# Kernel tuning notes

Measured on AMD Instinct MI355X. Metric: run time of the kernel, lower is better.

Reference implementation:

```python
import jax, jax.numpy as jnp
import numpy as np

# irreps_in == irreps_out == 512x0e + 256x1o + 128x2e
# each entry: (multiplicity, irrep dimension 2l+1)
IRREPS = [(512, 1), (256, 3), (128, 5)]
DIM_TOTAL = sum(m * d for m, d in IRREPS)          # 1920
WEIGHT_NUMEL = sum(m * m for m, _ in IRREPS)       # 344064
N = 16384


def setup_inputs() -> dict:
    key = jax.random.key(0)
    kx, kw = jax.random.split(key)
    x = jax.random.normal(kx, (N, DIM_TOTAL), dtype=jnp.float32)
    weight = jax.random.normal(kw, (WEIGHT_NUMEL,), dtype=jnp.float32)
    return {"x": x, "weight": weight}


def reference(x, weight):
    """Segmented (block-diagonal per irrep) linear mixing with 1/sqrt(fan_in) norm."""
    n = x.shape[0]
    outs = []
    x_off = 0
    w_off = 0
    for mul, d in IRREPS:
        seg = x[:, x_off:x_off + mul * d].reshape(n, mul, d)      # [N, mul, 2l+1]
        W = weight[w_off:w_off + mul * mul].reshape(mul, mul)     # [mul_in, mul_out]
        scale = jnp.asarray(1.0 / np.sqrt(mul), dtype=x.dtype)
        y = jnp.einsum('nui,uv->nvi', seg, W) * scale             # channel mix per component
        outs.append(y.reshape(n, mul * d))
        x_off += mul * d
        w_off += mul * mul
    return jnp.concatenate(outs, axis=-1)
```

## Files before the change

### kernel.cpp

```cpp
#include <hip/hip_runtime.h>


typedef float  f32x4  __attribute__((ext_vector_type(4)));
typedef short  bf16x8 __attribute__((ext_vector_type(8)));

#define ROWLEN 1920

__device__ __forceinline__ unsigned short f2bf(float f) {
    union { float f; unsigned int u; } c; c.f = f;
    unsigned int u = c.u;
    u += 0x7fffu + ((u >> 16) & 1u);
    return (unsigned short)(u >> 16);
}

__global__ __launch_bounds__(256) void prep_weights(const float* __restrict__ w,
                                                    unsigned short* __restrict__ wt) {
    int g = blockIdx.x * 256 + threadIdx.x;
    if (g >= 344064) return;
    int base, sh;
    if      (g < 262144) { base = 0;      sh = 9; }
    else if (g < 327680) { base = 262144; sh = 8; }
    else                 { base = 327680; sh = 7; }
    int local = g - base;
    int u = local >> sh;
    int v = local & ((1 << sh) - 1);
    wt[base + (v << sh) + u] = f2bf(w[g]);
}

template<int MUL, int D, int TN, int X_OFF, int WT_BASE>
__device__ __forceinline__ void seg_body(const int bid,
                                         const float* __restrict__ x,
                                         const unsigned short* __restrict__ wt,
                                         float* __restrict__ out,
                                         const float scale,
                                         unsigned short* lds) {
    constexpr int KB      = 32;
    constexpr int NSTEP   = MUL / KB;
    constexpr int M_LOG   = TN * D;
    constexpr int MT      = M_LOG / 16;
    constexpr int WAVE_NT = MUL / 64;
    constexpr int ST      = MUL + 8;
    constexpr int ROW_F4  = MUL * D / 4;
    constexpr int ITERS   = TN * ROW_F4 / 256;

    const int tid  = threadIdx.x;
    const int wave = tid >> 6;
    const int lane = tid & 63;
    const int q    = lane >> 4;
    const int t16  = lane & 15;
    const int n0   = bid * TN;

    const float* __restrict__ xblk = x + X_OFF + n0 * ROWLEN;

#pragma unroll 4
    for (int it = 0; it < ITERS; ++it) {
        const int idx = tid + it * 256;
        const int nl  = idx / ROW_F4;
        const int c4  = (idx - nl * ROW_F4) * 4;
        const f32x4 vv = *(const f32x4*)(xblk + nl * ROWLEN + c4);
        if (D == 1) {
            unsigned int lo = (unsigned int)f2bf(vv[0]) | ((unsigned int)f2bf(vv[1]) << 16);
            unsigned int hi = (unsigned int)f2bf(vv[2]) | ((unsigned int)f2bf(vv[3]) << 16);
            unsigned int* p = (unsigned int*)&lds[nl * ST + c4];
            p[0] = lo; p[1] = hi;
        } else {
#pragma unroll
            for (int e = 0; e < 4; ++e) {
                const int c = c4 + e;
                const int u = c / D;
                const int i = c - u * D;
                lds[(i * TN + nl) * ST + u] = f2bf(vv[e]);
            }
        }
    }

    f32x4 acc[MT][WAVE_NT];
#pragma unroll
    for (int a = 0; a < MT; ++a)
#pragma unroll
        for (int b = 0; b < WAVE_NT; ++b) acc[a][b] = (f32x4)0.0f;

    __syncthreads();

    const unsigned short* __restrict__ wblk = wt + WT_BASE;
    const int vbase = wave * (WAVE_NT * 16) + t16;

#pragma unroll 1
    for (int ks = 0; ks < NSTEP; ++ks) {
        bf16x8 afr[MT];
#pragma unroll
        for (int tm = 0; tm < MT; ++tm)
            afr[tm] = *(const bf16x8*)&lds[(16 * tm + t16) * ST + ks * KB + q * 8];
#pragma unroll
        for (int tv = 0; tv < WAVE_NT; ++tv) {
            const bf16x8 bfr = *(const bf16x8*)&wblk[(vbase + tv * 16) * MUL + ks * KB + q * 8];
#pragma unroll
            for (int tm = 0; tm < MT; ++tm)
                acc[tm][tv] = __builtin_amdgcn_mfma_f32_16x16x32_bf16(afr[tm], bfr, acc[tm][tv], 0, 0, 0);
        }
    }

#pragma unroll
    for (int tm = 0; tm < MT; ++tm) {
#pragma unroll
        for (int tv = 0; tv < WAVE_NT; ++tv) {
            const int v = vbase + tv * 16;
#pragma unroll
            for (int r = 0; r < 4; ++r) {
                const int rit  = q * 4 + r;
                const int lrow = 16 * tm + rit;
                const int i    = lrow / TN;
                const int nl   = lrow - i * TN;
                out[(n0 + nl) * ROWLEN + X_OFF + v * D + i] = acc[tm][tv][r] * scale;
            }
        }
    }
}

__global__ __launch_bounds__(256, 4) void fused_gemm(const float* __restrict__ x,
                                                     const unsigned short* __restrict__ wt,
                                                     float* __restrict__ out) {
    extern __shared__ unsigned short lds[];
    const int b = blockIdx.x;
    const int g = b / 5;
    const int r = b - g * 5;
    if (r == 0) {
        seg_body<512, 1, 32, 0, 0>(g, x, wt, out, 0.044194173824f, lds);
    } else if (r <= 2) {
        seg_body<256, 3, 16, 512, 262144>(g * 2 + (r - 1), x, wt, out, 0.0625f, lds);
    } else {
        seg_body<128, 5, 16, 1280, 327680>(g * 2 + (r - 3), x, wt, out, 0.088388347648f, lds);
    }
}

extern "C" void kernel_launch(void* const* d_in, const int* in_sizes, int n_in,
                              void* d_out, int out_size, void* d_ws, size_t ws_size,
                              hipStream_t stream) {
    const float* x = (const float*)d_in[0];
    const float* w = (const float*)d_in[1];
    float* out = (float*)d_out;
    unsigned short* wt = (unsigned short*)d_ws;

    hipLaunchKernelGGL(prep_weights, dim3((344064 + 255) / 256), dim3(256), 0, stream, w, wt);
    hipLaunchKernelGGL(fused_gemm, dim3(2560), dim3(256), 33280, stream, x, wt, out);
}
```

Measured before the change: 283.7 us.

## Pre-swizzle weights into MFMA fragment order and software-pipeline the K loop

The weight prep kernel now writes bf16 weights in the exact per-lane MFMA B-fragment order, so each lane in the GEMM loads one contiguous 16-byte chunk per tile instead of doing strided transposed reads. The K loop is double-buffered in registers: the next step's A and B fragments are loaded while the current MFMAs issue. The scalar segment tile shrinks from 32 to 16 rows, giving a uniform 3-block grouping, a larger grid and less LDS per block. This raises register pressure and halves weight reuse per block for the 0e segment.

```diff
diff --git a/kernel.cpp b/kernel.cpp
--- a/kernel.cpp
+++ b/kernel.cpp
@@ -15,16 +15,23 @@
 
 __global__ __launch_bounds__(256) void prep_weights(const float* __restrict__ w,
                                                     unsigned short* __restrict__ wt) {
-    int g = blockIdx.x * 256 + threadIdx.x;
-    if (g >= 344064) return;
-    int base, sh;
-    if      (g < 262144) { base = 0;      sh = 9; }
-    else if (g < 327680) { base = 262144; sh = 8; }
-    else                 { base = 327680; sh = 7; }
-    int local = g - base;
-    int u = local >> sh;
-    int v = local & ((1 << sh) - 1);
-    wt[base + (v << sh) + u] = f2bf(w[g]);
+    const int g = blockIdx.x * 256 + threadIdx.x;
+    if (g >= 43008) return;
+    int t, base, mul, lognstep;
+    if      (g < 32768) { t = g;         base = 0;      mul = 512; lognstep = 4; }
+    else if (g < 40960) { t = g - 32768; base = 262144; mul = 256; lognstep = 3; }
+    else                { t = g - 40960; base = 327680; mul = 128; lognstep = 2; }
+    const int lane = t & 63;
+    const int rest = t >> 6;
+    const int ks   = rest & ((1 << lognstep) - 1);
+    const int vt   = rest >> lognstep;
+    const int v    = vt * 16 + (lane & 15);
+    const int k0   = ks * 32 + (lane >> 4) * 8;
+    const float* __restrict__ src = w + base + k0 * mul + v;
+    bf16x8 vv;
+#pragma unroll
+    for (int j = 0; j < 8; ++j) vv[j] = (short)f2bf(src[j * mul]);
+    *(bf16x8*)&wt[base + t * 8] = vv;
 }
 
 template<int MUL, int D, int TN, int X_OFF, int WT_BASE>
@@ -42,6 +49,7 @@
     constexpr int ST      = MUL + 8;
     constexpr int ROW_F4  = MUL * D / 4;
     constexpr int ITERS   = TN * ROW_F4 / 256;
+    constexpr int TVS     = NSTEP * 512;
 
     const int tid  = threadIdx.x;
     const int wave = tid >> 6;
@@ -51,8 +59,21 @@
     const int n0   = bid * TN;
 
     const float* __restrict__ xblk = x + X_OFF + n0 * ROWLEN;
+    const unsigned short* __restrict__ wfrag =
+        wt + WT_BASE + (wave * WAVE_NT) * TVS + lane * 8;
 
-#pragma unroll 4
+    f32x4 acc[MT][WAVE_NT];
+#pragma unroll
+    for (int a = 0; a < MT; ++a)
+#pragma unroll
+        for (int b = 0; b < WAVE_NT; ++b) acc[a][b] = (f32x4)0.0f;
+
+    bf16x8 bfr[WAVE_NT];
+#pragma unroll
+    for (int tv = 0; tv < WAVE_NT; ++tv)
+        bfr[tv] = *(const bf16x8*)&wfrag[tv * TVS];
+
+#pragma unroll
     for (int it = 0; it < ITERS; ++it) {
         const int idx = tid + it * 256;
         const int nl  = idx / ROW_F4;
@@ -74,37 +95,43 @@
         }
     }
 
-    f32x4 acc[MT][WAVE_NT];
-#pragma unroll
-    for (int a = 0; a < MT; ++a)
-#pragma unroll
-        for (int b = 0; b < WAVE_NT; ++b) acc[a][b] = (f32x4)0.0f;
-
     __syncthreads();
 
-    const unsigned short* __restrict__ wblk = wt + WT_BASE;
-    const int vbase = wave * (WAVE_NT * 16) + t16;
+    bf16x8 afr[MT];
+#pragma unroll
+    for (int tm = 0; tm < MT; ++tm)
+        afr[tm] = *(const bf16x8*)&lds[(16 * tm + t16) * ST + q * 8];
 
-#pragma unroll 1
-    for (int ks = 0; ks < NSTEP; ++ks) {
-        bf16x8 afr[MT];
+#pragma unroll 2
+    for (int ks = 0; ks < NSTEP - 1; ++ks) {
+        bf16x8 bnx[WAVE_NT], anx[MT];
+#pragma unroll
+        for (int tv = 0; tv < WAVE_NT; ++tv)
+            bnx[tv] = *(const bf16x8*)&wfrag[tv * TVS + (ks + 1) * 512];
 #pragma unroll
         for (int tm = 0; tm < MT; ++tm)
-            afr[tm] = *(const bf16x8*)&lds[(16 * tm + t16) * ST + ks * KB + q * 8];
+            anx[tm] = *(const bf16x8*)&lds[(16 * tm + t16) * ST + (ks + 1) * KB + q * 8];
 #pragma unroll
-        for (int tv = 0; tv < WAVE_NT; ++tv) {
-            const bf16x8 bfr = *(const bf16x8*)&wblk[(vbase + tv * 16) * MUL + ks * KB + q * 8];
+        for (int tv = 0; tv < WAVE_NT; ++tv)
 #pragma unroll
             for (int tm = 0; tm < MT; ++tm)
-                acc[tm][tv] = __builtin_amdgcn_mfma_f32_16x16x32_bf16(afr[tm], bfr, acc[tm][tv], 0, 0, 0);
-        }
+                acc[tm][tv] = __builtin_amdgcn_mfma_f32_16x16x32_bf16(afr[tm], bfr[tv], acc[tm][tv], 0, 0, 0);
+#pragma unroll
+        for (int tv = 0; tv < WAVE_NT; ++tv) bfr[tv] = bnx[tv];
+#pragma unroll
+        for (int tm = 0; tm < MT; ++tm) afr[tm] = anx[tm];
     }
+#pragma unroll
+    for (int tv = 0; tv < WAVE_NT; ++tv)
+#pragma unroll
+        for (int tm = 0; tm < MT; ++tm)
+            acc[tm][tv] = __builtin_amdgcn_mfma_f32_16x16x32_bf16(afr[tm], bfr[tv], acc[tm][tv], 0, 0, 0);
 
 #pragma unroll
     for (int tm = 0; tm < MT; ++tm) {
 #pragma unroll
         for (int tv = 0; tv < WAVE_NT; ++tv) {
-            const int v = vbase + tv * 16;
+            const int v = wave * (WAVE_NT * 16) + t16 + tv * 16;
 #pragma unroll
             for (int r = 0; r < 4; ++r) {
                 const int rit  = q * 4 + r;
@@ -122,14 +149,14 @@
                                                      float* __restrict__ out) {
     extern __shared__ unsigned short lds[];
     const int b = blockIdx.x;
-    const int g = b / 5;
-    const int r = b - g * 5;
+    const int g = b / 3;
+    const int r = b - g * 3;
     if (r == 0) {
-        seg_body<512, 1, 32, 0, 0>(g, x, wt, out, 0.044194173824f, lds);
-    } else if (r <= 2) {
-        seg_body<256, 3, 16, 512, 262144>(g * 2 + (r - 1), x, wt, out, 0.0625f, lds);
+        seg_body<512, 1, 16, 0, 0>(g, x, wt, out, 0.044194173824f, lds);
+    } else if (r == 1) {
+        seg_body<256, 3, 16, 512, 262144>(g, x, wt, out, 0.0625f, lds);
     } else {
-        seg_body<128, 5, 16, 1280, 327680>(g * 2 + (r - 3), x, wt, out, 0.088388347648f, lds);
+        seg_body<128, 5, 16, 1280, 327680>(g, x, wt, out, 0.088388347648f, lds);
     }
 }
 
@@ -141,6 +168,6 @@
     float* out = (float*)d_out;
     unsigned short* wt = (unsigned short*)d_ws;
 
-    hipLaunchKernelGGL(prep_weights, dim3((344064 + 255) / 256), dim3(256), 0, stream, w, wt);
-    hipLaunchKernelGGL(fused_gemm, dim3(2560), dim3(256), 33280, stream, x, wt, out);
+    hipLaunchKernelGGL(prep_weights, dim3(168), dim3(256), 0, stream, w, wt);
+    hipLaunchKernelGGL(fused_gemm, dim3(3072), dim3(256), 25344, stream, x, wt, out);
 }
```

Result: faster. 251.6 us (-11.3%).

## Pre-swizzle weights into MFMA fragment order, use 8 waves, prefetch B fragments

Applied to the files above, without the earlier changes.

The weight prep kernel now writes bf16 weights in per-lane MFMA fragment order, so each wave's B-operand load is a contiguous 16-byte-per-lane read. Blocks grow from 4 to 8 waves, which halves the output columns each wave handles. B fragments are loaded into registers before the x tile is staged to LDS, so the global weight latency overlaps the staging. When a wave's fragments fit they are all kept in registers; otherwise a 3-deep software prefetch is used. The trade-off is higher register pressure at 512 threads with launch_bounds(512,4), and occupancy may drop.

```diff
diff --git a/kernel.cpp b/kernel.cpp
--- a/kernel.cpp
+++ b/kernel.cpp
@@ -15,16 +15,21 @@
 
 __global__ __launch_bounds__(256) void prep_weights(const float* __restrict__ w,
                                                     unsigned short* __restrict__ wt) {
-    int g = blockIdx.x * 256 + threadIdx.x;
+    const int g = blockIdx.x * 256 + threadIdx.x;
     if (g >= 344064) return;
-    int base, sh;
-    if      (g < 262144) { base = 0;      sh = 9; }
-    else if (g < 327680) { base = 262144; sh = 8; }
-    else                 { base = 327680; sh = 7; }
-    int local = g - base;
-    int u = local >> sh;
-    int v = local & ((1 << sh) - 1);
-    wt[base + (v << sh) + u] = f2bf(w[g]);
+    int base, lmul;
+    if      (g < 262144) { base = 0;      lmul = 9; }
+    else if (g < 327680) { base = 262144; lmul = 8; }
+    else                 { base = 327680; lmul = 7; }
+    const int local = g - base;
+    const int u = local >> lmul;
+    const int v = local & ((1 << lmul) - 1);
+    const int nstep_log = lmul - 5;
+    const int vt   = v >> 4;
+    const int ks   = u >> 5;
+    const int lane = (((u >> 3) & 3) << 4) | (v & 15);
+    const int j    = u & 7;
+    wt[base + ((((vt << nstep_log) + ks) << 6) + lane) * 8 + j] = f2bf(w[g]);
 }
 
 template<int MUL, int D, int TN, int X_OFF, int WT_BASE>
@@ -38,10 +43,13 @@
     constexpr int NSTEP   = MUL / KB;
     constexpr int M_LOG   = TN * D;
     constexpr int MT      = M_LOG / 16;
-    constexpr int WAVE_NT = MUL / 64;
+    constexpr int NWAVE   = 8;
+    constexpr int WAVE_NT = MUL / (NWAVE * 16);
     constexpr int ST      = MUL + 8;
     constexpr int ROW_F4  = MUL * D / 4;
-    constexpr int ITERS   = TN * ROW_F4 / 256;
+    constexpr int ITERS   = TN * ROW_F4 / (NWAVE * 64);
+    constexpr int TVS     = NSTEP * 512;
+    constexpr bool BREG   = (WAVE_NT * NSTEP) <= 16;
 
     const int tid  = threadIdx.x;
     const int wave = tid >> 6;
@@ -51,28 +59,8 @@
     const int n0   = bid * TN;
 
     const float* __restrict__ xblk = x + X_OFF + n0 * ROWLEN;
-
-#pragma unroll 4
-    for (int it = 0; it < ITERS; ++it) {
-        const int idx = tid + it * 256;
-        const int nl  = idx / ROW_F4;
-        const int c4  = (idx - nl * ROW_F4) * 4;
-        const f32x4 vv = *(const f32x4*)(xblk + nl * ROWLEN + c4);
-        if (D == 1) {
-            unsigned int lo = (unsigned int)f2bf(vv[0]) | ((unsigned int)f2bf(vv[1]) << 16);
-            unsigned int hi = (unsigned int)f2bf(vv[2]) | ((unsigned int)f2bf(vv[3]) << 16);
-            unsigned int* p = (unsigned int*)&lds[nl * ST + c4];
-            p[0] = lo; p[1] = hi;
-        } else {
-#pragma unroll
-            for (int e = 0; e < 4; ++e) {
-                const int c = c4 + e;
-                const int u = c / D;
-                const int i = c - u * D;
-                lds[(i * TN + nl) * ST + u] = f2bf(vv[e]);
-            }
-        }
-    }
+    const unsigned short* __restrict__ wfrag =
+        wt + WT_BASE + (wave * WAVE_NT) * TVS + lane * 8;
 
     f32x4 acc[MT][WAVE_NT];
 #pragma unroll
@@ -80,23 +68,77 @@
 #pragma unroll
         for (int b = 0; b < WAVE_NT; ++b) acc[a][b] = (f32x4)0.0f;
 
-    __syncthreads();
+    auto stage_tile = [&]() {
+#pragma unroll
+        for (int it = 0; it < ITERS; ++it) {
+            const int idx = tid + it * (NWAVE * 64);
+            const int nl  = idx / ROW_F4;
+            const int c4  = (idx - nl * ROW_F4) * 4;
+            const f32x4 vv = *(const f32x4*)(xblk + nl * ROWLEN + c4);
+            if (D == 1) {
+                unsigned int lo = (unsigned int)f2bf(vv[0]) | ((unsigned int)f2bf(vv[1]) << 16);
+                unsigned int hi = (unsigned int)f2bf(vv[2]) | ((unsigned int)f2bf(vv[3]) << 16);
+                unsigned int* p = (unsigned int*)&lds[nl * ST + c4];
+                p[0] = lo; p[1] = hi;
+            } else {
+#pragma unroll
+                for (int e = 0; e < 4; ++e) {
+                    const int c = c4 + e;
+                    const int u = c / D;
+                    const int i = c - u * D;
+                    lds[(i * TN + nl) * ST + u] = f2bf(vv[e]);
+                }
+            }
+        }
+    };
 
-    const unsigned short* __restrict__ wblk = wt + WT_BASE;
-    const int vbase = wave * (WAVE_NT * 16) + t16;
-
-#pragma unroll 1
-    for (int ks = 0; ks < NSTEP; ++ks) {
-        bf16x8 afr[MT];
+    if constexpr (BREG) {
+        bf16x8 breg[WAVE_NT * NSTEP];
 #pragma unroll
-        for (int tm = 0; tm < MT; ++tm)
-            afr[tm] = *(const bf16x8*)&lds[(16 * tm + t16) * ST + ks * KB + q * 8];
+        for (int tv = 0; tv < WAVE_NT; ++tv)
 #pragma unroll
-        for (int tv = 0; tv < WAVE_NT; ++tv) {
-            const bf16x8 bfr = *(const bf16x8*)&wblk[(vbase + tv * 16) * MUL + ks * KB + q * 8];
+            for (int ks = 0; ks < NSTEP; ++ks)
+                breg[tv * NSTEP + ks] = *(const bf16x8*)&wfrag[tv * TVS + ks * 512];
+        stage_tile();
+        __syncthreads();
+#pragma unroll
+        for (int ks = 0; ks < NSTEP; ++ks) {
+            bf16x8 afr[MT];
 #pragma unroll
             for (int tm = 0; tm < MT; ++tm)
-                acc[tm][tv] = __builtin_amdgcn_mfma_f32_16x16x32_bf16(afr[tm], bfr, acc[tm][tv], 0, 0, 0);
+                afr[tm] = *(const bf16x8*)&lds[(16 * tm + t16) * ST + ks * KB + q * 8];
+#pragma unroll
+            for (int tv = 0; tv < WAVE_NT; ++tv)
+#pragma unroll
+                for (int tm = 0; tm < MT; ++tm)
+                    acc[tm][tv] = __builtin_amdgcn_mfma_f32_16x16x32_bf16(afr[tm], breg[tv * NSTEP + ks], acc[tm][tv], 0, 0, 0);
+        }
+    } else {
+        constexpr int PF = 3;
+        bf16x8 bfr[4][WAVE_NT];
+#pragma unroll
+        for (int p = 0; p < PF; ++p)
+#pragma unroll
+            for (int tv = 0; tv < WAVE_NT; ++tv)
+                bfr[p][tv] = *(const bf16x8*)&wfrag[tv * TVS + p * 512];
+        stage_tile();
+        __syncthreads();
+#pragma unroll
+        for (int ks = 0; ks < NSTEP; ++ks) {
+            if (ks + PF < NSTEP) {
+#pragma unroll
+                for (int tv = 0; tv < WAVE_NT; ++tv)
+                    bfr[(ks + PF) & 3][tv] = *(const bf16x8*)&wfrag[tv * TVS + (ks + PF) * 512];
+            }
+            bf16x8 afr[MT];
+#pragma unroll
+            for (int tm = 0; tm < MT; ++tm)
+                afr[tm] = *(const bf16x8*)&lds[(16 * tm + t16) * ST + ks * KB + q * 8];
+#pragma unroll
+            for (int tv = 0; tv < WAVE_NT; ++tv)
+#pragma unroll
+                for (int tm = 0; tm < MT; ++tm)
+                    acc[tm][tv] = __builtin_amdgcn_mfma_f32_16x16x32_bf16(afr[tm], bfr[ks & 3][tv], acc[tm][tv], 0, 0, 0);
         }
     }
 
@@ -104,7 +146,7 @@
     for (int tm = 0; tm < MT; ++tm) {
 #pragma unroll
         for (int tv = 0; tv < WAVE_NT; ++tv) {
-            const int v = vbase + tv * 16;
+            const int v = wave * (WAVE_NT * 16) + t16 + tv * 16;
 #pragma unroll
             for (int r = 0; r < 4; ++r) {
                 const int rit  = q * 4 + r;
@@ -117,7 +159,7 @@
     }
 }
 
-__global__ __launch_bounds__(256, 4) void fused_gemm(const float* __restrict__ x,
+__global__ __launch_bounds__(512, 4) void fused_gemm(const float* __restrict__ x,
                                                      const unsigned short* __restrict__ wt,
                                                      float* __restrict__ out) {
     extern __shared__ unsigned short lds[];
@@ -141,6 +183,6 @@
     float* out = (float*)d_out;
     unsigned short* wt = (unsigned short*)d_ws;
 
-    hipLaunchKernelGGL(prep_weights, dim3((344064 + 255) / 256), dim3(256), 0, stream, w, wt);
-    hipLaunchKernelGGL(fused_gemm, dim3(2560), dim3(256), 33280, stream, x, wt, out);
+    hipLaunchKernelGGL(prep_weights, dim3(1344), dim3(256), 0, stream, w, wt);
+    hipLaunchKernelGGL(fused_gemm, dim3(2560), dim3(512), 33280, stream, x, wt, out);
 }
```

After: 235.8 us. 1.2x faster.

## Double-buffer K-sliced A/B tiles in LDS with async global-to-LDS weight loads

Applied to the files above, without the earlier changes.

Restructures the fused segmented GEMM into a K-step pipeline. Each 32-wide K slice of x (converted to bf16) and of the weights is staged into double-buffered LDS, so the next slice loads while the current one feeds MFMA. Weights are pre-swizzled into an MFMA-fragment-major layout and copied with global_load_lds. The kernel also moves to 512-thread blocks with a 2D wave tiling, larger row tiles and N-blocking, giving a different grid decomposition. This adds a barrier per K step and more LDS per block (48 KB), which may reduce occupancy.

```diff
diff --git a/kernel.cpp b/kernel.cpp
--- a/kernel.cpp
+++ b/kernel.cpp
@@ -13,123 +13,171 @@
     return (unsigned short)(u >> 16);
 }
 
+__device__ __forceinline__ void gload_lds16(const unsigned short* g, unsigned short* l) {
+    __builtin_amdgcn_global_load_lds(
+        (const __attribute__((address_space(1))) unsigned int*)g,
+        (__attribute__((address_space(3))) unsigned int*)l, 16, 0, 0);
+}
+
 __global__ __launch_bounds__(256) void prep_weights(const float* __restrict__ w,
                                                     unsigned short* __restrict__ wt) {
-    int g = blockIdx.x * 256 + threadIdx.x;
+    const int g = blockIdx.x * 256 + threadIdx.x;
     if (g >= 344064) return;
-    int base, sh;
-    if      (g < 262144) { base = 0;      sh = 9; }
-    else if (g < 327680) { base = 262144; sh = 8; }
-    else                 { base = 327680; sh = 7; }
-    int local = g - base;
-    int u = local >> sh;
-    int v = local & ((1 << sh) - 1);
-    wt[base + (v << sh) + u] = f2bf(w[g]);
+    int base, lmul;
+    if      (g < 262144) { base = 0;      lmul = 9; }
+    else if (g < 327680) { base = 262144; lmul = 8; }
+    else                 { base = 327680; lmul = 7; }
+    const int local = g - base;
+    const int u = local >> lmul;
+    const int v = local & ((1 << lmul) - 1);
+    const int NSUB = 1 << (lmul - 4);
+    const int ks   = u >> 5;
+    const int nsub = v >> 4;
+    const int lane = (((u >> 3) & 3) << 4) | (v & 15);
+    const int j    = u & 7;
+    wt[base + ((ks * NSUB + nsub) * 64 + lane) * 8 + j] = f2bf(w[g]);
 }
 
-template<int MUL, int D, int TN, int X_OFF, int WT_BASE>
-__device__ __forceinline__ void seg_body(const int bid,
+template<int MUL, int D, int TN, int BN, int X_OFF, int WT_BASE, int WROWS>
+__device__ __forceinline__ void seg_body(const int wid,
                                          const float* __restrict__ x,
                                          const unsigned short* __restrict__ wt,
                                          float* __restrict__ out,
                                          const float scale,
                                          unsigned short* lds) {
-    constexpr int KB      = 32;
-    constexpr int NSTEP   = MUL / KB;
-    constexpr int M_LOG   = TN * D;
-    constexpr int MT      = M_LOG / 16;
-    constexpr int WAVE_NT = MUL / 64;
-    constexpr int ST      = MUL + 8;
-    constexpr int ROW_F4  = MUL * D / 4;
-    constexpr int ITERS   = TN * ROW_F4 / 256;
+    constexpr int NSTEP    = MUL / 32;
+    constexpr int M_LOG    = TN * D;
+    constexpr int WCOLS    = 8 / WROWS;
+    constexpr int MT       = M_LOG / (16 * WROWS);
+    constexpr int NT       = BN / (16 * WCOLS);
+    constexpr int NSUB_WG  = BN / 16;
+    constexpr int NSUB_SEG = MUL / 16;
+    constexpr int NB       = MUL / BN;
+    constexpr int ST       = 40;
+    constexpr int A_BUF    = M_LOG * ST;
+    constexpr int B_BUF    = NSUB_WG * 512;
+    constexpr int F4S      = TN * 8 * D;
+    constexpr int SWEEPS   = (F4S + 511) / 512;
+    constexpr int BCALLS   = NSUB_WG / 8;
 
-    const int tid  = threadIdx.x;
-    const int wave = tid >> 6;
-    const int lane = tid & 63;
-    const int q    = lane >> 4;
-    const int t16  = lane & 15;
-    const int n0   = bid * TN;
+    const int tid    = threadIdx.x;
+    const int wave   = tid >> 6;
+    const int lane   = tid & 63;
+    const int q      = lane >> 4;
+    const int t16    = lane & 15;
+    const int wg_m   = wid / NB;
+    const int nb     = wid - wg_m * NB;
+    const int n0     = wg_m * TN;
+    const int wave_r = wave / WCOLS;
+    const int wave_c = wave - wave_r * WCOLS;
 
-    const float* __restrict__ xblk = x + X_OFF + n0 * ROWLEN;
+    const float* __restrict__ xbase = x + X_OFF + n0 * ROWLEN;
+    unsigned short* __restrict__ Alds = lds;
+    unsigned short* __restrict__ Blds = lds + 2 * A_BUF;
 
-#pragma unroll 4
-    for (int it = 0; it < ITERS; ++it) {
-        const int idx = tid + it * 256;
-        const int nl  = idx / ROW_F4;
-        const int c4  = (idx - nl * ROW_F4) * 4;
-        const f32x4 vv = *(const f32x4*)(xblk + nl * ROWLEN + c4);
-        if (D == 1) {
-            unsigned int lo = (unsigned int)f2bf(vv[0]) | ((unsigned int)f2bf(vv[1]) << 16);
-            unsigned int hi = (unsigned int)f2bf(vv[2]) | ((unsigned int)f2bf(vv[3]) << 16);
-            unsigned int* p = (unsigned int*)&lds[nl * ST + c4];
-            p[0] = lo; p[1] = hi;
-        } else {
+    auto stage_B = [&](int buf, int ks) {
+        const unsigned short* __restrict__ slab =
+            wt + WT_BASE + (ks * NSUB_SEG + nb * NSUB_WG) * 512;
+        unsigned short* __restrict__ Bl = Blds + buf * B_BUF;
 #pragma unroll
-            for (int e = 0; e < 4; ++e) {
-                const int c = c4 + e;
-                const int u = c / D;
-                const int i = c - u * D;
-                lds[(i * TN + nl) * ST + u] = f2bf(vv[e]);
+        for (int c = 0; c < BCALLS; ++c) {
+            const int blk = wave * BCALLS + c;
+            gload_lds16(slab + blk * 512 + lane * 8, Bl + blk * 512);
+        }
+    };
+
+    auto stage_A = [&](int buf, int ks) {
+        unsigned short* __restrict__ Al = Alds + buf * A_BUF;
+        const float* __restrict__ src = xbase + ks * 32 * D;
+#pragma unroll
+        for (int s = 0; s < SWEEPS; ++s) {
+            const int fi = s * 512 + tid;
+            if ((F4S % 512 == 0) || (fi < F4S)) {
+                const int nl = fi / (8 * D);
+                const int c4 = (fi - nl * (8 * D)) * 4;
+                const f32x4 vv = *(const f32x4*)(src + nl * ROWLEN + c4);
+                if (D == 1) {
+                    unsigned int lo = (unsigned int)f2bf(vv[0]) | ((unsigned int)f2bf(vv[1]) << 16);
+                    unsigned int hi = (unsigned int)f2bf(vv[2]) | ((unsigned int)f2bf(vv[3]) << 16);
+                    unsigned int* p = (unsigned int*)&Al[nl * ST + c4];
+                    p[0] = lo; p[1] = hi;
+                } else {
+#pragma unroll
+                    for (int e = 0; e < 4; ++e) {
+                        const int c = c4 + e;
+                        const int u = c / D;
+                        const int i = c - u * D;
+                        Al[(i * TN + nl) * ST + u] = f2bf(vv[e]);
+                    }
+                }
             }
         }
-    }
+    };
 
-    f32x4 acc[MT][WAVE_NT];
+    f32x4 acc[MT][NT];
 #pragma unroll
     for (int a = 0; a < MT; ++a)
 #pragma unroll
-        for (int b = 0; b < WAVE_NT; ++b) acc[a][b] = (f32x4)0.0f;
+        for (int b = 0; b < NT; ++b) acc[a][b] = (f32x4)0.0f;
 
+    stage_B(0, 0);
+    stage_A(0, 0);
     __syncthreads();
 
-    const unsigned short* __restrict__ wblk = wt + WT_BASE;
-    const int vbase = wave * (WAVE_NT * 16) + t16;
+    const int arow0  = wave_r * (MT * 16) + t16;
+    const int nsub0  = wave_c * NT;
 
-#pragma unroll 1
+#pragma unroll 2
     for (int ks = 0; ks < NSTEP; ++ks) {
-        bf16x8 afr[MT];
+        const int cur = ks & 1, nxt = cur ^ 1;
+        if (ks + 1 < NSTEP) stage_B(nxt, ks + 1);
+        const unsigned short* __restrict__ Al = Alds + cur * A_BUF;
+        const unsigned short* __restrict__ Bl = Blds + cur * B_BUF;
+        bf16x8 afr[MT], bfr[NT];
 #pragma unroll
         for (int tm = 0; tm < MT; ++tm)
-            afr[tm] = *(const bf16x8*)&lds[(16 * tm + t16) * ST + ks * KB + q * 8];
+            afr[tm] = *(const bf16x8*)&Al[(arow0 + tm * 16) * ST + q * 8];
 #pragma unroll
-        for (int tv = 0; tv < WAVE_NT; ++tv) {
-            const bf16x8 bfr = *(const bf16x8*)&wblk[(vbase + tv * 16) * MUL + ks * KB + q * 8];
+        for (int tv = 0; tv < NT; ++tv)
+            bfr[tv] = *(const bf16x8*)&Bl[(nsub0 + tv) * 512 + lane * 8];
+        if (ks + 1 < NSTEP) stage_A(nxt, ks + 1);
+#pragma unroll
+        for (int tv = 0; tv < NT; ++tv)
 #pragma unroll
             for (int tm = 0; tm < MT; ++tm)
-                acc[tm][tv] = __builtin_amdgcn_mfma_f32_16x16x32_bf16(afr[tm], bfr, acc[tm][tv], 0, 0, 0);
-        }
+                acc[tm][tv] = __builtin_amdgcn_mfma_f32_16x16x32_bf16(afr[tm], bfr[tv], acc[tm][tv], 0, 0, 0);
+        __syncthreads();
     }
 
+    const int vcol0 = nb * BN + wave_c * (NT * 16) + t16;
 #pragma unroll
     for (int tm = 0; tm < MT; ++tm) {
 #pragma unroll
-        for (int tv = 0; tv < WAVE_NT; ++tv) {
-            const int v = vbase + tv * 16;
+        for (int tv = 0; tv < NT; ++tv) {
 #pragma unroll
             for (int r = 0; r < 4; ++r) {
-                const int rit  = q * 4 + r;
-                const int lrow = 16 * tm + rit;
+                const int lrow = wave_r * (MT * 16) + tm * 16 + q * 4 + r;
                 const int i    = lrow / TN;
                 const int nl   = lrow - i * TN;
-                out[(n0 + nl) * ROWLEN + X_OFF + v * D + i] = acc[tm][tv][r] * scale;
+                out[(n0 + nl) * ROWLEN + X_OFF + (vcol0 + tv * 16) * D + i] = acc[tm][tv][r] * scale;
             }
         }
     }
 }
 
-__global__ __launch_bounds__(256, 4) void fused_gemm(const float* __restrict__ x,
+__global__ __launch_bounds__(512, 4) void fused_gemm(const float* __restrict__ x,
                                                      const unsigned short* __restrict__ wt,
                                                      float* __restrict__ out) {
     extern __shared__ unsigned short lds[];
     const int b = blockIdx.x;
-    const int g = b / 5;
-    const int r = b - g * 5;
+    const int wid = b / 3;
+    const int r = b - wid * 3;
     if (r == 0) {
-        seg_body<512, 1, 32, 0, 0>(g, x, wt, out, 0.044194173824f, lds);
-    } else if (r <= 2) {
-        seg_body<256, 3, 16, 512, 262144>(g * 2 + (r - 1), x, wt, out, 0.0625f, lds);
+        seg_body<512, 1, 64, 256, 0, 0, 1>(wid, x, wt, out, 0.044194173824f, lds);
+    } else if (r == 1) {
+        seg_body<256, 3, 32, 256, 512, 262144, 2>(wid, x, wt, out, 0.0625f, lds);
     } else {
-        seg_body<128, 5, 16, 1280, 327680>(g * 2 + (r - 3), x, wt, out, 0.088388347648f, lds);
+        seg_body<128, 5, 32, 128, 1280, 327680, 2>(wid, x, wt, out, 0.088388347648f, lds);
     }
 }
 
@@ -141,6 +189,6 @@
     float* out = (float*)d_out;
     unsigned short* wt = (unsigned short*)d_ws;
 
-    hipLaunchKernelGGL(prep_weights, dim3((344064 + 255) / 256), dim3(256), 0, stream, w, wt);
-    hipLaunchKernelGGL(fused_gemm, dim3(2560), dim3(256), 33280, stream, x, wt, out);
+    hipLaunchKernelGGL(prep_weights, dim3(1344), dim3(256), 0, stream, w, wt);
+    hipLaunchKernelGGL(fused_gemm, dim3(1536), dim3(512), 48128, stream, x, wt, out);
 }
```

After: 252.0 us. 1.13x faster.
